# Kernel optimization log

Measured on AMD Instinct MI355X. Metric: run time of the kernel, lower is better.

Reference implementation:

```python
import jax, jax.numpy as jnp
import numpy as np

DIM = 768
NUM_HEADS = 12
HEAD_DIM = DIM // NUM_HEADS
HIDDEN = int(DIM * 4.0)
EPS = 1e-8


def layer_norm(x, w, b):
    mu = jnp.mean(x, axis=-1, keepdims=True)
    var = jnp.mean(jnp.square(x - mu), axis=-1, keepdims=True)
    return (x - mu) * jax.lax.rsqrt(var + EPS) * w + b


def setup_inputs() -> dict:
    key = jax.random.key(0)
    ks = jax.random.split(key, 10)
    s = 0.02
    return {
        "x": jax.random.normal(ks[0], (16, 4096, DIM), dtype=jnp.float32),
        # Linear weights stored as [in, out]
        "qkv_w": jax.random.normal(ks[1], (DIM, 3 * DIM), dtype=jnp.float32) * s,
        "qkv_b": jnp.zeros((3 * DIM,), dtype=jnp.float32),
        "proj_w": jax.random.normal(ks[2], (DIM, DIM), dtype=jnp.float32) * s,
        "proj_b": jnp.zeros((DIM,), dtype=jnp.float32),
        "fc1_w": jax.random.normal(ks[3], (DIM, HIDDEN), dtype=jnp.float32) * s,
        "fc1_b": jnp.zeros((HIDDEN,), dtype=jnp.float32),
        "fc2_w": jax.random.normal(ks[4], (HIDDEN, DIM), dtype=jnp.float32) * s,
        "fc2_b": jnp.zeros((DIM,), dtype=jnp.float32),
        "ln1_w": jnp.ones((DIM,), dtype=jnp.float32),
        "ln1_b": jnp.zeros((DIM,), dtype=jnp.float32),
        "ln2_w": jnp.ones((DIM,), dtype=jnp.float32),
        "ln2_b": jnp.zeros((DIM,), dtype=jnp.float32),
    }


def linear_attention(x, qkv_w, qkv_b, proj_w, proj_b):
    B, N, C = x.shape
    qkv = (x @ qkv_w + qkv_b).reshape(B, N, 3, NUM_HEADS, HEAD_DIM)
    qkv = qkv.transpose(2, 0, 3, 1, 4)  # [3, B, H, N, D]
    q, k, v = qkv[0], qkv[1], qkv[2]
    q = jax.nn.elu(q) + 1.0
    k = jax.nn.elu(k) + 1.0
    kv = jnp.einsum('bhsd,bhse->bhde', k, v)          # [B,H,D,D]
    z = 1.0 / jnp.einsum('bhsd,bhd->bhs', q, k.sum(axis=-2))  # [B,H,N]
    out = jnp.einsum('bhde,bhsd,bhs->bhse', kv, q, z)  # [B,H,N,D]
    out = out.transpose(0, 2, 1, 3).reshape(B, N, C)
    return out @ proj_w + proj_b


def reference(x, qkv_w, qkv_b, proj_w, proj_b, fc1_w, fc1_b, fc2_w, fc2_b,
              ln1_w, ln1_b, ln2_w, ln2_b):
    y = linear_attention(layer_norm(x, ln1_w, ln1_b), qkv_w, qkv_b, proj_w, proj_b)
    x = x + y
    h = layer_norm(x, ln2_w, ln2_b)
    h = jax.nn.gelu(h @ fc1_w + fc1_b, approximate=False) @ fc2_w + fc2_b
    return x + h
```

## Files before the change

kernel.cpp:

```cpp
#include <hip/hip_runtime.h>

#define DEVI __device__ __forceinline__

typedef __attribute__((ext_vector_type(8))) short bf16x8;
typedef __attribute__((ext_vector_type(4))) float f32x4;
typedef __attribute__((ext_vector_type(4))) unsigned short usx4;

DEVI float bf2f(unsigned short u) {
  unsigned int b = ((unsigned int)u) << 16;
  float f;
  __builtin_memcpy(&f, &b, 4);
  return f;
}
DEVI unsigned short f2bf(float f) {
  unsigned int x;
  __builtin_memcpy(&x, &f, 4);
  x += 0x7FFFu + ((x >> 16) & 1u);
  return (unsigned short)(x >> 16);
}
DEVI void gload_lds16(const void* g, void* l) {
  __builtin_amdgcn_global_load_lds((const __attribute__((address_space(1))) void*)g,
                                   (__attribute__((address_space(3))) void*)l,
                                   16, 0, 0);
}
DEVI float gelu_fast(float x) {
  const float u = 0.7978845608028654f * (x + 0.044715f * x * x * x);
  const float a = fabsf(u);
  const float e = __expf(-2.0f * a);
  float th = __fdividef(1.0f - e, 1.0f + e);
  th = u < 0.f ? -th : th;
  return 0.5f * x * (1.0f + th);
}

__global__ __launch_bounds__(256) void wt_kernel(const float* __restrict__ W,
                                                 unsigned short* __restrict__ Wt,
                                                 int K, int N) {
  __shared__ float t[32][33];
  const int tx = threadIdx.x & 31, ty = threadIdx.x >> 5;
  const int n0 = blockIdx.x * 32, k0 = blockIdx.y * 32;
#pragma unroll
  for (int i = 0; i < 4; ++i)
    t[ty * 4 + i][tx] = W[(size_t)(k0 + ty * 4 + i) * N + n0 + tx];
  __syncthreads();
#pragma unroll
  for (int i = 0; i < 4; ++i)
    Wt[(size_t)(n0 + ty * 4 + i) * K + k0 + tx] = f2bf(t[tx][ty * 4 + i]);
}

__global__ __launch_bounds__(256) void ln_kernel(const float* __restrict__ x,
                                                 const float* __restrict__ w,
                                                 const float* __restrict__ b,
                                                 unsigned short* __restrict__ o) {
  const int lane = threadIdx.x & 63;
  const int wave = threadIdx.x >> 6;
  const size_t row = (size_t)blockIdx.x * 4 + wave;
  const float* xr = x + row * 768;
  float v[12];
  float s = 0.f, sq = 0.f;
#pragma unroll
  for (int i = 0; i < 3; ++i) {
    const float4 f = *(const float4*)&xr[i * 256 + lane * 4];
    v[i * 4 + 0] = f.x; v[i * 4 + 1] = f.y; v[i * 4 + 2] = f.z; v[i * 4 + 3] = f.w;
    s += f.x + f.y + f.z + f.w;
    sq += f.x * f.x + f.y * f.y + f.z * f.z + f.w * f.w;
  }
#pragma unroll
  for (int off = 32; off > 0; off >>= 1) {
    s += __shfl_xor(s, off);
    sq += __shfl_xor(sq, off);
  }
  const float mu = s * (1.f / 768.f);
  const float rs = rsqrtf(sq * (1.f / 768.f) - mu * mu + 1e-8f);
  unsigned short* orow = o + row * 768;
#pragma unroll
  for (int i = 0; i < 3; ++i) {
    usx4 st;
#pragma unroll
    for (int j = 0; j < 4; ++j) {
      const int c = i * 256 + lane * 4 + j;
      st[j] = f2bf((v[i * 4 + j] - mu) * rs * w[c] + b[c]);
    }
    *(usx4*)&orow[i * 256 + lane * 4] = st;
  }
}

__global__ __launch_bounds__(256) void fuse_kernel(const float* __restrict__ x,
                                                   const unsigned short* __restrict__ y,
                                                   const float* __restrict__ w,
                                                   const float* __restrict__ b,
                                                   float* __restrict__ x2,
                                                   unsigned short* __restrict__ o) {
  const int lane = threadIdx.x & 63;
  const int wave = threadIdx.x >> 6;
  const size_t row = (size_t)blockIdx.x * 4 + wave;
  const float* xr = x + row * 768;
  const unsigned short* yr = y + row * 768;
  float* x2r = x2 + row * 768;
  float v[12];
  float s = 0.f, sq = 0.f;
#pragma unroll
  for (int i = 0; i < 3; ++i) {
    const float4 f = *(const float4*)&xr[i * 256 + lane * 4];
    const usx4 yv = *(const usx4*)&yr[i * 256 + lane * 4];
    float t0 = f.x + bf2f(yv[0]);
    float t1 = f.y + bf2f(yv[1]);
    float t2 = f.z + bf2f(yv[2]);
    float t3 = f.w + bf2f(yv[3]);
    v[i * 4 + 0] = t0; v[i * 4 + 1] = t1; v[i * 4 + 2] = t2; v[i * 4 + 3] = t3;
    s += t0 + t1 + t2 + t3;
    sq += t0 * t0 + t1 * t1 + t2 * t2 + t3 * t3;
    float4 fo; fo.x = t0; fo.y = t1; fo.z = t2; fo.w = t3;
    *(float4*)&x2r[i * 256 + lane * 4] = fo;
  }
#pragma unroll
  for (int off = 32; off > 0; off >>= 1) {
    s += __shfl_xor(s, off);
    sq += __shfl_xor(sq, off);
  }
  const float mu = s * (1.f / 768.f);
  const float rs = rsqrtf(sq * (1.f / 768.f) - mu * mu + 1e-8f);
  unsigned short* orow = o + row * 768;
#pragma unroll
  for (int i = 0; i < 3; ++i) {
    usx4 st;
#pragma unroll
    for (int j = 0; j < 4; ++j) {
      const int c = i * 256 + lane * 4 + j;
      st[j] = f2bf((v[i * 4 + j] - mu) * rs * w[c] + b[c]);
    }
    *(usx4*)&orow[i * 256 + lane * 4] = st;
  }
}

template <int EPI>
__global__ __launch_bounds__(512, 4) void gemm_k(
    const unsigned short* __restrict__ A, const unsigned short* __restrict__ Bt,
    const float* __restrict__ bias, int N, int K,
    unsigned short* __restrict__ O0, unsigned short* __restrict__ O1,
    unsigned short* __restrict__ O2, float* __restrict__ OF) {
  __shared__ unsigned short sm[24576];
  const int tid = threadIdx.x;
  const int lane = tid & 63, wave = tid >> 6;
  const int wr = wave >> 2, wc = wave & 3;

  const int gx = gridDim.x;
  const int nwg = gx * gridDim.y;
  const int cpx = nwg >> 3;
  const int wgid = blockIdx.x + gx * blockIdx.y;
  const int v = (wgid & 7) * cpx + (wgid >> 3);
  const size_t n0 = (size_t)(v % gx) * 256;
  const size_t m0 = (size_t)(v / gx) * 128;

  const int rA = tid >> 2;
  const int cA = (tid & 3) ^ ((rA ^ (rA >> 2)) & 3);
  const unsigned short* srcA = A + (m0 + rA) * (size_t)K + cA * 8;
  const unsigned short* srcB0 = Bt + (n0 + rA) * (size_t)K + cA * 8;
  const unsigned short* srcB1 = srcB0 + (size_t)128 * K;

  unsigned short* smA = sm;
  unsigned short* smB = sm + 8192;

  f32x4 acc[4][4];
#pragma unroll
  for (int m = 0; m < 4; ++m)
#pragma unroll
    for (int n = 0; n < 4; ++n) acc[m][n] = f32x4{0.f, 0.f, 0.f, 0.f};

  const int L = lane & 15, kc4 = lane >> 4;
  const int fL = (L ^ (L >> 2)) & 3;
  const int aoff = (wr * 64 + L) * 32 + ((kc4 ^ fL) << 3);
  const int boff = (wc * 64 + L) * 32 + ((kc4 ^ fL) << 3);

  const int nt = K >> 5;

#define STAGE(tt)                                              \
  do {                                                         \
    const int p_ = (tt) & 1;                                   \
    const size_t ko_ = (size_t)(tt) * 32;                      \
    gload_lds16(srcA + ko_, smA + p_ * 4096 + tid * 8);        \
    gload_lds16(srcB0 + ko_, smB + p_ * 8192 + tid * 8);       \
    gload_lds16(srcB1 + ko_, smB + p_ * 8192 + 4096 + tid * 8);\
  } while (0)

  STAGE(0);
  STAGE(1);

  for (int t = 0; t < nt; ++t) {
    if (t + 1 < nt)
      asm volatile("s_waitcnt vmcnt(3)" ::: "memory");
    else
      asm volatile("s_waitcnt vmcnt(0)" ::: "memory");
    __builtin_amdgcn_s_barrier();
    const unsigned short* Abase = smA + (t & 1) * 4096 + aoff;
    const unsigned short* Bbase = smB + (t & 1) * 8192 + boff;
    bf16x8 aF[4], bF[4];
#pragma unroll
    for (int m = 0; m < 4; ++m) aF[m] = *(const bf16x8*)(Abase + m * 512);
#pragma unroll
    for (int n = 0; n < 4; ++n) bF[n] = *(const bf16x8*)(Bbase + n * 512);
    asm volatile("s_waitcnt lgkmcnt(0)" ::: "memory");
    __builtin_amdgcn_s_barrier();
    if (t + 2 < nt) STAGE(t + 2);
    __builtin_amdgcn_s_setprio(1);
#pragma unroll
    for (int m = 0; m < 4; ++m)
#pragma unroll
      for (int n = 0; n < 4; ++n)
        acc[m][n] = __builtin_amdgcn_mfma_f32_16x16x32_bf16(aF[m], bF[n], acc[m][n], 0, 0, 0);
    __builtin_amdgcn_s_setprio(0);
  }
#undef STAGE

  const int rl = (lane >> 4) * 4;
  const int cl = lane & 15;

  if (EPI == 2) {
    const int cbase = (int)n0 + wc * 64;
    const int tsec = cbase / 768;
    const int h = (cbase - tsec * 768) >> 6;
    const int rbase = (int)m0 + wr * 64;
    const int b = rbase >> 12;
    const int s0w = rbase & 4095;
    const size_t bh = (size_t)b * 12 + h;
    unsigned short* dst = (tsec == 0) ? O0 : (tsec == 1 ? O1 : O2);
#pragma unroll
    for (int m = 0; m < 4; ++m)
#pragma unroll
      for (int n = 0; n < 4; ++n) {
        const int d = n * 16 + cl;
        const float bv = bias[cbase + d];
#pragma unroll
        for (int j = 0; j < 4; ++j) {
          float val = acc[m][n][j] + bv;
          if (tsec < 2) val = val > 0.f ? val + 1.f : __expf(val);
          dst[(bh * 4096 + (size_t)(s0w + m * 16 + rl + j)) * 64 + d] = f2bf(val);
        }
      }
    return;
  }

#pragma unroll
  for (int m = 0; m < 4; ++m) {
    const size_t r0 = m0 + wr * 64 + m * 16 + rl;
#pragma unroll
    for (int n = 0; n < 4; ++n) {
      const size_t c = n0 + wc * 64 + n * 16 + cl;
      const float bv = bias[c];
      if (EPI == 0) {
#pragma unroll
        for (int j = 0; j < 4; ++j) O0[(r0 + j) * (size_t)N + c] = f2bf(acc[m][n][j] + bv);
      } else if (EPI == 1) {
#pragma unroll
        for (int j = 0; j < 4; ++j) {
          O0[(r0 + j) * (size_t)N + c] = f2bf(gelu_fast(acc[m][n][j] + bv));
        }
      } else {
#pragma unroll
        for (int j = 0; j < 4; ++j) {
          const size_t idx = (r0 + j) * (size_t)N + c;
          OF[idx] += acc[m][n][j] + bv;
        }
      }
    }
  }
}

__global__ __launch_bounds__(256) void kv_kernel(const unsigned short* __restrict__ k,
                                                 const unsigned short* __restrict__ v,
                                                 float* __restrict__ kvT,
                                                 float* __restrict__ ksum) {
  __shared__ unsigned short kl[8192];
  __shared__ unsigned short vl[8192];
  __shared__ float red[256];
  const int tid = threadIdx.x, lane = tid & 63, wave = tid >> 6;
  const size_t bh = blockIdx.x;
  const unsigned short* kb = k + bh * (size_t)(4096 * 64);
  const unsigned short* vb = v + bh * (size_t)(4096 * 64);
  f32x4 acc[4];
#pragma unroll
  for (int n = 0; n < 4; ++n) acc[n] = f32x4{0.f, 0.f, 0.f, 0.f};
  float ks = 0.f;

  const int r = tid >> 1;
  const int hf = tid & 1;
  const int c4 = r >> 5;
  const int scw = (r >> 3) & 3;
  int wofs[4];
#pragma unroll
  for (int dd = 0; dd < 4; ++dd)
    wofs[dd] = c4 * 32 + ((scw ^ ((c4 ^ dd) & 3)) << 3) + (r & 7);

  const int L = lane & 15, kc4 = lane >> 4;
  const int dA = wave * 16 + L;
  const int dq = tid & 63, q4 = tid >> 6;
  const int Fks = (q4 ^ dq) & 3;
  const int ksbase = (dq * 4 + q4) * 32;

  for (int st = 0; st < 32; ++st) {
    const int s0 = st * 128;
    __syncthreads();
    {
      const unsigned short* krow = kb + (size_t)(s0 + r) * 64 + hf * 32;
      const unsigned short* vrow = vb + (size_t)(s0 + r) * 64 + hf * 32;
      bf16x8 kk[4], vv[4];
#pragma unroll
      for (int g = 0; g < 4; ++g) {
        kk[g] = *(const bf16x8*)(krow + g * 8);
        vv[g] = *(const bf16x8*)(vrow + g * 8);
      }
#pragma unroll
      for (int g = 0; g < 4; ++g)
#pragma unroll
        for (int i = 0; i < 8; ++i) {
          const int d = hf * 32 + g * 8 + i;
          const int a = d * 128 + wofs[d & 3];
          kl[a] = (unsigned short)kk[g][i];
          vl[a] = (unsigned short)vv[g][i];
        }
    }
    __syncthreads();
#pragma unroll
    for (int scc = 0; scc < 4; ++scc) {
      const bf16x8 t8 = *(const bf16x8*)&kl[ksbase + ((scc ^ Fks) << 3)];
#pragma unroll
      for (int i = 0; i < 8; ++i) ks += bf2f((unsigned short)t8[i]);
    }
#pragma unroll
    for (int ksl = 0; ksl < 4; ++ksl) {
      const int physA = kc4 ^ ((ksl ^ dA) & 3);
      const bf16x8 aF = *(const bf16x8*)&kl[(dA * 4 + ksl) * 32 + physA * 8];
#pragma unroll
      for (int n = 0; n < 4; ++n) {
        const int e = n * 16 + L;
        const int physB = kc4 ^ ((ksl ^ e) & 3);
        const bf16x8 bF = *(const bf16x8*)&vl[(e * 4 + ksl) * 32 + physB * 8];
        acc[n] = __builtin_amdgcn_mfma_f32_16x16x32_bf16(aF, bF, acc[n], 0, 0, 0);
      }
    }
  }
  red[tid] = ks;
  __syncthreads();
  if (tid < 64) ksum[bh * 64 + tid] = red[tid] + red[64 + tid] + red[128 + tid] + red[192 + tid];
#pragma unroll
  for (int n = 0; n < 4; ++n)
#pragma unroll
    for (int j = 0; j < 4; ++j) {
      const int d = wave * 16 + (lane >> 4) * 4 + j;
      const int e = n * 16 + (lane & 15);
      kvT[bh * 4096 + e * 64 + d] = acc[n][j];
    }
}

__global__ __launch_bounds__(256) void attn_out_kernel(const unsigned short* __restrict__ q,
                                                       const float* __restrict__ kvT,
                                                       const float* __restrict__ ksum,
                                                       unsigned short* __restrict__ attnout) {
  __shared__ float kvl[4096];
  __shared__ float ksl[64];
  __shared__ float zl[4 * 64];
  const int tid = threadIdx.x;
  const int lane = tid & 63, wave = tid >> 6;
  const int bh = blockIdx.x >> 2;
  const int chunk = blockIdx.x & 3;
  const int b = bh / 12, h = bh % 12;
  const float* kvb = kvT + (size_t)bh * 4096;
  for (int i = tid; i < 4096; i += 256) kvl[i] = kvb[i];
  if (tid < 64) ksl[tid] = ksum[(size_t)bh * 64 + tid];
  __syncthreads();

  const int kh = (lane >> 4) * 8;
  bf16x8 bF[4], ksF;
#pragma unroll
  for (int n = 0; n < 4; ++n) {
    bf16x8 t;
#pragma unroll
    for (int j = 0; j < 8; ++j)
      t[j] = (short)f2bf(kvl[((lane & 15) + 16 * n) * 64 + kh + j]);
    bF[n] = t;
  }
  {
    bf16x8 t;
#pragma unroll
    for (int j = 0; j < 8; ++j)
      t[j] = ((lane & 15) == 0) ? (short)f2bf(ksl[kh + j]) : (short)0;
    ksF = t;
  }
  const unsigned short* qb = q + (size_t)bh * 4096 * 64;

  for (int st = 0; st < 4; ++st) {
    const int s0 = chunk * 1024 + wave * 256 + st * 64;
    bf16x8 aF[4];
#pragma unroll
    for (int m = 0; m < 4; ++m)
      aF[m] = *(const bf16x8*)&qb[(size_t)(s0 + (lane & 15) + 16 * m) * 64 + kh];
    f32x4 acc[4][4];
    f32x4 dacc[4];
#pragma unroll
    for (int m = 0; m < 4; ++m) {
      dacc[m] = f32x4{0.f, 0.f, 0.f, 0.f};
#pragma unroll
      for (int n = 0; n < 4; ++n) acc[m][n] = f32x4{0.f, 0.f, 0.f, 0.f};
    }
#pragma unroll
    for (int m = 0; m < 4; ++m) {
#pragma unroll
      for (int n = 0; n < 4; ++n)
        acc[m][n] = __builtin_amdgcn_mfma_f32_16x16x32_bf16(aF[m], bF[n], acc[m][n], 0, 0, 0);
      dacc[m] = __builtin_amdgcn_mfma_f32_16x16x32_bf16(aF[m], ksF, dacc[m], 0, 0, 0);
    }
    if ((lane & 15) == 0) {
#pragma unroll
      for (int m = 0; m < 4; ++m)
#pragma unroll
        for (int j = 0; j < 4; ++j)
          zl[wave * 64 + m * 16 + (lane >> 4) * 4 + j] = 1.0f / dacc[m][j];
    }
    __syncthreads();
#pragma unroll
    for (int m = 0; m < 4; ++m)
#pragma unroll
      for (int n = 0; n < 4; ++n)
#pragma unroll
        for (int j = 0; j < 4; ++j) {
          const int sl = m * 16 + (lane >> 4) * 4 + j;
          const int s = s0 + sl;
          const float val = acc[m][n][j] * zl[wave * 64 + sl];
          const int e = n * 16 + (lane & 15);
          attnout[((size_t)b * 4096 + s) * 768 + h * 64 + e] = f2bf(val);
        }
    __syncthreads();
  }
}

extern "C" void kernel_launch(void* const* d_in, const int* in_sizes, int n_in,
                              void* d_out, int out_size, void* d_ws, size_t ws_size,
                              hipStream_t stream) {
  const float* x = (const float*)d_in[0];
  const float* qkv_w = (const float*)d_in[1];
  const float* qkv_b = (const float*)d_in[2];
  const float* proj_w = (const float*)d_in[3];
  const float* proj_b = (const float*)d_in[4];
  const float* fc1_w = (const float*)d_in[5];
  const float* fc1_b = (const float*)d_in[6];
  const float* fc2_w = (const float*)d_in[7];
  const float* fc2_b = (const float*)d_in[8];
  const float* ln1_w = (const float*)d_in[9];
  const float* ln1_b = (const float*)d_in[10];
  const float* ln2_w = (const float*)d_in[11];
  const float* ln2_b = (const float*)d_in[12];
  float* out = (float*)d_out;

  char* ws = (char*)d_ws;
  const size_t PL = (size_t)65536 * 768 * 2;
  unsigned short* xn = (unsigned short*)(ws + 0 * PL);
  unsigned short* q = (unsigned short*)(ws + 1 * PL);
  unsigned short* kbuf = (unsigned short*)(ws + 2 * PL);
  unsigned short* vbuf = (unsigned short*)(ws + 3 * PL);
  unsigned short* attnout = xn;
  unsigned short* ybuf = kbuf;
  unsigned short* xn2 = (unsigned short*)(ws + 4 * PL);
  unsigned short* hbuf = (unsigned short*)(ws + 0 * PL);
  size_t off = 5 * PL;
  float* kvT = (float*)(ws + off); off += (size_t)192 * 4096 * 4;
  float* ksum = (float*)(ws + off); off += (size_t)192 * 64 * 4;
  unsigned short* qkvWt = (unsigned short*)(ws + off); off += (size_t)2304 * 768 * 2;
  unsigned short* projWt = (unsigned short*)(ws + off); off += (size_t)768 * 768 * 2;
  unsigned short* fc1Wt = (unsigned short*)(ws + off); off += (size_t)3072 * 768 * 2;
  unsigned short* fc2Wt = (unsigned short*)(ws + off); off += (size_t)768 * 3072 * 2;

  wt_kernel<<<dim3(72, 24), 256, 0, stream>>>(qkv_w, qkvWt, 768, 2304);
  wt_kernel<<<dim3(24, 24), 256, 0, stream>>>(proj_w, projWt, 768, 768);
  wt_kernel<<<dim3(96, 24), 256, 0, stream>>>(fc1_w, fc1Wt, 768, 3072);
  wt_kernel<<<dim3(24, 96), 256, 0, stream>>>(fc2_w, fc2Wt, 3072, 768);
  ln_kernel<<<16384, 256, 0, stream>>>(x, ln1_w, ln1_b, xn);
  gemm_k<2><<<dim3(9, 512), 512, 0, stream>>>(xn, qkvWt, qkv_b, 2304, 768, q, kbuf, vbuf, nullptr);
  kv_kernel<<<192, 256, 0, stream>>>(kbuf, vbuf, kvT, ksum);
  attn_out_kernel<<<768, 256, 0, stream>>>(q, kvT, ksum, attnout);
  gemm_k<0><<<dim3(3, 512), 512, 0, stream>>>(attnout, projWt, proj_b, 768, 768, ybuf, nullptr,
                                              nullptr, nullptr);
  fuse_kernel<<<16384, 256, 0, stream>>>(x, ybuf, ln2_w, ln2_b, out, xn2);
  gemm_k<1><<<dim3(12, 512), 512, 0, stream>>>(xn2, fc1Wt, fc1_b, 3072, 768, hbuf, nullptr,
                                               nullptr, nullptr);
  gemm_k<3><<<dim3(3, 512), 512, 0, stream>>>(hbuf, fc2Wt, fc2_b, 768, 3072, nullptr, nullptr,
                                              nullptr, out);
  (void)in_sizes; (void)n_in; (void)out_size; (void)ws_size;
}
```

Before: 1.538 ms.

## Triple-buffer GEMM loads, transpose MFMA for vector epilogue stores, reverse block order

The GEMM moves from double to triple buffering in LDS, keeping three K-tiles of global loads in flight, with vmcnt waits adjusted to match. The MFMA operands are swapped so each lane holds four consecutive output columns, which lets the epilogues use float4 bias loads and 4-wide bf16/fp32 stores instead of scalar strided stores. Block order is reversed in the fc2 GEMM and in the kv and attn_out kernels, so data the previous kernel wrote last, and that is likely still in L2, gets read first. The larger LDS footprint may lower how many workgroups fit on each CU.

```diff
diff --git a/kernel.cpp b/kernel.cpp
--- a/kernel.cpp
+++ b/kernel.cpp
@@ -138,7 +138,7 @@
     const float* __restrict__ bias, int N, int K,
     unsigned short* __restrict__ O0, unsigned short* __restrict__ O1,
     unsigned short* __restrict__ O2, float* __restrict__ OF) {
-  __shared__ unsigned short sm[24576];
+  __shared__ unsigned short sm[36864];
   const int tid = threadIdx.x;
   const int lane = tid & 63, wave = tid >> 6;
   const int wr = wave >> 2, wc = wave & 3;
@@ -146,7 +146,8 @@
   const int gx = gridDim.x;
   const int nwg = gx * gridDim.y;
   const int cpx = nwg >> 3;
-  const int wgid = blockIdx.x + gx * blockIdx.y;
+  int wgid = blockIdx.x + gx * blockIdx.y;
+  if (EPI == 3) wgid = nwg - 1 - wgid;
   const int v = (wgid & 7) * cpx + (wgid >> 3);
   const size_t n0 = (size_t)(v % gx) * 256;
   const size_t m0 = (size_t)(v / gx) * 128;
@@ -158,7 +159,7 @@
   const unsigned short* srcB1 = srcB0 + (size_t)128 * K;
 
   unsigned short* smA = sm;
-  unsigned short* smB = sm + 8192;
+  unsigned short* smB = sm + 12288;
 
   f32x4 acc[4][4];
 #pragma unroll
@@ -173,26 +174,30 @@
 
   const int nt = K >> 5;
 
-#define STAGE(tt)                                              \
-  do {                                                         \
-    const int p_ = (tt) & 1;                                   \
-    const size_t ko_ = (size_t)(tt) * 32;                      \
-    gload_lds16(srcA + ko_, smA + p_ * 4096 + tid * 8);        \
-    gload_lds16(srcB0 + ko_, smB + p_ * 8192 + tid * 8);       \
-    gload_lds16(srcB1 + ko_, smB + p_ * 8192 + 4096 + tid * 8);\
+#define STAGE(tt)                                               \
+  do {                                                          \
+    const int p_ = (tt) % 3;                                    \
+    const size_t ko_ = (size_t)(tt) * 32;                       \
+    gload_lds16(srcA + ko_, smA + p_ * 4096 + tid * 8);         \
+    gload_lds16(srcB0 + ko_, smB + p_ * 8192 + tid * 8);        \
+    gload_lds16(srcB1 + ko_, smB + p_ * 8192 + 4096 + tid * 8); \
   } while (0)
 
   STAGE(0);
   STAGE(1);
+  STAGE(2);
 
   for (int t = 0; t < nt; ++t) {
-    if (t + 1 < nt)
+    const int rem = nt - t;
+    if (rem > 2)
+      asm volatile("s_waitcnt vmcnt(6)" ::: "memory");
+    else if (rem == 2)
       asm volatile("s_waitcnt vmcnt(3)" ::: "memory");
     else
       asm volatile("s_waitcnt vmcnt(0)" ::: "memory");
     __builtin_amdgcn_s_barrier();
-    const unsigned short* Abase = smA + (t & 1) * 4096 + aoff;
-    const unsigned short* Bbase = smB + (t & 1) * 8192 + boff;
+    const unsigned short* Abase = smA + (t % 3) * 4096 + aoff;
+    const unsigned short* Bbase = smB + (t % 3) * 8192 + boff;
     bf16x8 aF[4], bF[4];
 #pragma unroll
     for (int m = 0; m < 4; ++m) aF[m] = *(const bf16x8*)(Abase + m * 512);
@@ -200,19 +205,19 @@
     for (int n = 0; n < 4; ++n) bF[n] = *(const bf16x8*)(Bbase + n * 512);
     asm volatile("s_waitcnt lgkmcnt(0)" ::: "memory");
     __builtin_amdgcn_s_barrier();
-    if (t + 2 < nt) STAGE(t + 2);
+    if (t + 3 < nt) STAGE(t + 3);
     __builtin_amdgcn_s_setprio(1);
 #pragma unroll
     for (int m = 0; m < 4; ++m)
 #pragma unroll
       for (int n = 0; n < 4; ++n)
-        acc[m][n] = __builtin_amdgcn_mfma_f32_16x16x32_bf16(aF[m], bF[n], acc[m][n], 0, 0, 0);
+        acc[m][n] = __builtin_amdgcn_mfma_f32_16x16x32_bf16(bF[n], aF[m], acc[m][n], 0, 0, 0);
     __builtin_amdgcn_s_setprio(0);
   }
 #undef STAGE
 
-  const int rl = (lane >> 4) * 4;
   const int cl = lane & 15;
+  const int cg = (lane >> 4) * 4;
 
   if (EPI == 2) {
     const int cbase = (int)n0 + wc * 64;
@@ -224,42 +229,50 @@
     const size_t bh = (size_t)b * 12 + h;
     unsigned short* dst = (tsec == 0) ? O0 : (tsec == 1 ? O1 : O2);
 #pragma unroll
-    for (int m = 0; m < 4; ++m)
+    for (int m = 0; m < 4; ++m) {
+      const size_t s = (size_t)(s0w + m * 16 + cl);
 #pragma unroll
       for (int n = 0; n < 4; ++n) {
-        const int d = n * 16 + cl;
-        const float bv = bias[cbase + d];
+        const int d0 = n * 16 + cg;
+        const float4 bv = *(const float4*)&bias[cbase + d0];
+        usx4 st;
 #pragma unroll
         for (int j = 0; j < 4; ++j) {
-          float val = acc[m][n][j] + bv;
+          float val = acc[m][n][j] + ((const float*)&bv)[j];
           if (tsec < 2) val = val > 0.f ? val + 1.f : __expf(val);
-          dst[(bh * 4096 + (size_t)(s0w + m * 16 + rl + j)) * 64 + d] = f2bf(val);
+          st[j] = f2bf(val);
         }
+        *(usx4*)&dst[(bh * 4096 + s) * 64 + d0] = st;
       }
+    }
     return;
   }
 
 #pragma unroll
   for (int m = 0; m < 4; ++m) {
-    const size_t r0 = m0 + wr * 64 + m * 16 + rl;
+    const size_t r = m0 + wr * 64 + m * 16 + cl;
 #pragma unroll
     for (int n = 0; n < 4; ++n) {
-      const size_t c = n0 + wc * 64 + n * 16 + cl;
-      const float bv = bias[c];
+      const size_t c = n0 + wc * 64 + n * 16 + cg;
+      const float4 bv = *(const float4*)&bias[c];
       if (EPI == 0) {
-#pragma unroll
-        for (int j = 0; j < 4; ++j) O0[(r0 + j) * (size_t)N + c] = f2bf(acc[m][n][j] + bv);
+        usx4 st;
+#pragma unroll
+        for (int j = 0; j < 4; ++j) st[j] = f2bf(acc[m][n][j] + ((const float*)&bv)[j]);
+        *(usx4*)&O0[r * (size_t)N + c] = st;
       } else if (EPI == 1) {
-#pragma unroll
-        for (int j = 0; j < 4; ++j) {
-          O0[(r0 + j) * (size_t)N + c] = f2bf(gelu_fast(acc[m][n][j] + bv));
-        }
+        usx4 st;
+#pragma unroll
+        for (int j = 0; j < 4; ++j)
+          st[j] = f2bf(gelu_fast(acc[m][n][j] + ((const float*)&bv)[j]));
+        *(usx4*)&O0[r * (size_t)N + c] = st;
       } else {
-#pragma unroll
-        for (int j = 0; j < 4; ++j) {
-          const size_t idx = (r0 + j) * (size_t)N + c;
-          OF[idx] += acc[m][n][j] + bv;
-        }
+        float4 o = *(const float4*)&OF[r * (size_t)N + c];
+        o.x += acc[m][n][0] + bv.x;
+        o.y += acc[m][n][1] + bv.y;
+        o.z += acc[m][n][2] + bv.z;
+        o.w += acc[m][n][3] + bv.w;
+        *(float4*)&OF[r * (size_t)N + c] = o;
       }
     }
   }
@@ -273,7 +286,7 @@
   __shared__ unsigned short vl[8192];
   __shared__ float red[256];
   const int tid = threadIdx.x, lane = tid & 63, wave = tid >> 6;
-  const size_t bh = blockIdx.x;
+  const size_t bh = (size_t)(gridDim.x - 1 - blockIdx.x);
   const unsigned short* kb = k + bh * (size_t)(4096 * 64);
   const unsigned short* vb = v + bh * (size_t)(4096 * 64);
   f32x4 acc[4];
@@ -360,8 +373,9 @@
   __shared__ float zl[4 * 64];
   const int tid = threadIdx.x;
   const int lane = tid & 63, wave = tid >> 6;
-  const int bh = blockIdx.x >> 2;
-  const int chunk = blockIdx.x & 3;
+  const int bidx = gridDim.x - 1 - blockIdx.x;
+  const int bh = bidx >> 2;
+  const int chunk = bidx & 3;
   const int b = bh / 12, h = bh % 12;
   const float* kvb = kvT + (size_t)bh * 4096;
   for (int i = tid; i < 4096; i += 256) kvl[i] = kvb[i];
```

After: 1.556 ms. No clear change (+1.2%).
